# Kernel tuning notes

Measured on AMD Instinct MI355X. Metric: run time of the kernel, lower is better.

## Reference

```python
import jax, jax.numpy as jnp
import numpy as np

# irrep blocks for 0e+1o+2e: dims 1, 3, 5 (total D=9)
BLOCKS = [(0, 1), (1, 4), (4, 9)]

def block_linear(x, W):
    # x: [N, C, 9], W: [3, C, C] -- e3nn Linear mixes channels within each irrep block
    outs = [jnp.einsum('ncd,cq->nqd', x[..., s:e], W[l]) for l, (s, e) in enumerate(BLOCKS)]
    return jnp.concatenate(outs, axis=-1)

def setup_inputs() -> dict:
    key = jax.random.key(0)
    ks = jax.random.split(key, 14)
    N, E, C, D, B, H, Z = 16384, 262144, 32, 9, 8, 64, 4
    inp = {
        'node_feats': jax.random.normal(ks[0], (N, C, D), jnp.float32),
        'node_attrs': jax.random.uniform(ks[1], (N, Z), jnp.float32),
        'edge_feats': jax.random.normal(ks[2], (E, B), jnp.float32),
        'edge_sh': jax.random.normal(ks[3], (E, D), jnp.float32),
        'cutoff': jax.random.uniform(ks[4], (E, 1), jnp.float32),
        # learned params
        'W_up': jax.random.normal(ks[5], (3, C, C), jnp.float32) / np.float32(np.sqrt(C)),
        'W1': jax.random.normal(ks[6], (B, H), jnp.float32) / np.float32(np.sqrt(B)),
        'W2': jax.random.normal(ks[7], (H, H), jnp.float32) / np.float32(np.sqrt(H)),
        'W3': jax.random.normal(ks[8], (H, C), jnp.float32) / np.float32(np.sqrt(H)),
        'W_lin': jax.random.normal(ks[9], (3, C, C), jnp.float32) / np.float32(np.sqrt(C)),
        'W_sc': jax.random.normal(ks[10], (Z, 3, C, C), jnp.float32) / np.float32(np.sqrt(C)),
        # fixed Clebsch-Gordan-like coupling tensor (constant structure of the TP)
        'CG': jax.random.normal(ks[11], (D, D, D), jnp.float32) / np.float32(D),
        'edge_src': jax.random.randint(ks[12], (E,), 0, N, jnp.int32),
        'edge_dst': jax.random.randint(ks[13], (E,), 0, N, jnp.int32),
    }
    return inp

def reference(node_feats, node_attrs, edge_feats, edge_sh, cutoff,
              W_up, W1, W2, W3, W_lin, W_sc, CG, edge_src, edge_dst):
    N = node_feats.shape[0]
    avg_num_neighbors = 16.0
    # linear_up: per-irrep channel mixing
    x = block_linear(node_feats, W_up)
    # radial MLP -> per-edge tensor-product weights, gated by cutoff
    h = jax.nn.silu(edge_feats @ W1)
    h = jax.nn.silu(h @ W2)
    w = (h @ W3) * cutoff  # [E, C]
    # gather source node feats, weighted equivariant tensor product per edge
    xs = x[edge_src]  # [E, C, D]
    m_ij = jnp.einsum('eci,ej,ijk,ec->eck', xs, edge_sh, CG, w)  # [E, C, D]
    # scatter-sum aggregation into destination nodes
    m_i = jax.ops.segment_sum(m_ij, edge_dst, num_segments=N)  # [N, C, D]
    # output linear + neighbor normalization
    m_i = block_linear(m_i, W_lin) / avg_num_neighbors
    # element-dependent self-connection from current message
    W_node = jnp.einsum('nz,zlcq->nlcq', node_attrs, W_sc)  # [N, 3, C, C]
    scs = jnp.concatenate(
        [jnp.einsum('ncd,ncq->nqd', m_i[..., s:e], W_node[:, l]) for l, (s, e) in enumerate(BLOCKS)],
        axis=-1)
    return (m_i, scs)
```

## Files before the change

kernel.cpp:

```cpp
#include <hip/hip_runtime.h>
#include <cstdint>

#define CC 32
#define DD 9
#define CD 288
#define BB 8
#define HH 64
#define ZZ 4
#define NB 8

typedef __attribute__((ext_vector_type(8))) short bf16x8;
typedef __attribute__((ext_vector_type(4))) float f32x4;
typedef __attribute__((ext_vector_type(2))) float f32x2;

__device__ __forceinline__ float silu_f(float v) {
  return v / (1.0f + __expf(-v));
}

__device__ __forceinline__ int blk_of(int d) { return d == 0 ? 0 : (d < 4 ? 1 : 2); }

__device__ __forceinline__ unsigned int f2bf(float f) {
  unsigned int u = __float_as_uint(f);
  return (u + 0x7fffu + ((u >> 16) & 1u)) >> 16;
}
__device__ __forceinline__ float bf_lo(unsigned int u) { return __uint_as_float(u << 16); }
__device__ __forceinline__ float bf_hi(unsigned int u) { return __uint_as_float(u & 0xffff0000u); }

__global__ __launch_bounds__(256) void k_zero(float* __restrict__ p, int n) {
  int i = blockIdx.x * 256 + threadIdx.x;
  if (i < n) p[i] = 0.0f;
}

__global__ __launch_bounds__(256) void k_hist(const int* __restrict__ edst,
                                              int* __restrict__ deg, int E) {
  int e = blockIdx.x * 256 + threadIdx.x;
  if (e < E) atomicAdd(&deg[edst[e]], 1);
}

__global__ __launch_bounds__(1024) void k_scan(const int* __restrict__ deg,
                                               int* __restrict__ offs,
                                               int* __restrict__ cursor, int N) {
  __shared__ int part[1024];
  int t = threadIdx.x;
  int chunk = (N + 1023) >> 10;
  int base = t * chunk;
  int lim = N - base; if (lim > chunk) lim = chunk; if (lim < 0) lim = 0;
  int s = 0;
  for (int i = 0; i < lim; ++i) s += deg[base + i];
  part[t] = s;
  __syncthreads();
  for (int off = 1; off < 1024; off <<= 1) {
    int v = part[t];
    int u = (t >= off) ? part[t - off] : 0;
    __syncthreads();
    part[t] = v + u;
    __syncthreads();
  }
  int run = (t == 0) ? 0 : part[t - 1];
  for (int i = 0; i < lim; ++i) {
    offs[base + i] = run;
    cursor[base + i] = run;
    run += deg[base + i];
  }
  if (t == 1023) offs[N] = run;
}

__global__ __launch_bounds__(256) void k_scatter(const int* __restrict__ edst,
                                                 const int* __restrict__ esrc,
                                                 const float* __restrict__ esh,
                                                 int* __restrict__ cursor,
                                                 int* __restrict__ eidx,
                                                 int* __restrict__ srcs,
                                                 unsigned int* __restrict__ esh_p, int E) {
  int e = blockIdx.x * 256 + threadIdx.x;
  if (e < E) {
    int d = edst[e];
    int pos = atomicAdd(&cursor[d], 1);
    eidx[pos] = e;
    srcs[pos] = esrc[e];
    const float* sp = esh + (size_t)e * 9;
    unsigned int* op = esh_p + (size_t)pos * 5;
#pragma unroll
    for (int jj = 0; jj < 5; ++jj) {
      unsigned int lo = f2bf(sp[2 * jj]);
      unsigned int hi = (jj < 4) ? f2bf(sp[2 * jj + 1]) : 0u;
      op[jj] = lo | (hi << 16);
    }
  }
}

__global__ __launch_bounds__(288) void k_linear_up(
    const float* __restrict__ nf, const float* __restrict__ Wup,
    unsigned int* __restrict__ x_p, int N) {
  __shared__ float snf[NB][DD * 36];
  __shared__ float sval[NB][DD][CC];
  int t = threadIdx.x;
  int g = t >> 5, q = t & 31;
  int tc = t / 9, td = t - tc * 9;
  int l0 = blk_of(g);
  float wcol[CC];
#pragma unroll
  for (int c = 0; c < CC; ++c) wcol[c] = Wup[l0 * 1024 + c * 32 + q];
  int n0 = blockIdx.x * NB;
#pragma unroll
  for (int nb = 0; nb < NB; ++nb) {
    if (n0 + nb < N) snf[nb][td * 36 + tc] = nf[(size_t)(n0 + nb) * CD + t];
  }
  __syncthreads();
#pragma unroll
  for (int nb = 0; nb < NB; ++nb) {
    if (n0 + nb >= N) break;
    const float4* rowp = (const float4*)(snf[nb] + g * 36);
    float a0 = 0.f, a1 = 0.f;
#pragma unroll
    for (int c4 = 0; c4 < 8; ++c4) {
      float4 b = rowp[c4];
      a0 += b.x * wcol[c4 * 4 + 0] + b.y * wcol[c4 * 4 + 1];
      a1 += b.z * wcol[c4 * 4 + 2] + b.w * wcol[c4 * 4 + 3];
    }
    sval[nb][g][q] = a0 + a1;
  }
  __syncthreads();
#pragma unroll
  for (int it = 0; it < 5; ++it) {
    int idx = it * 288 + t;
    if (idx < NB * 160) {
      int nb = idx / 160, r = idx - nb * 160;
      int p = r >> 5, c = r & 31;
      if (n0 + nb < N) {
        unsigned int lo = f2bf(sval[nb][2 * p][c]);
        unsigned int hi = (p < 4) ? f2bf(sval[nb][2 * p + 1][c]) : 0u;
        x_p[(size_t)(n0 + nb) * 160 + r] = lo | (hi << 16);
      }
    }
  }
}

__global__ __launch_bounds__(64) void k_mlp_mfma(
    const float* __restrict__ ef, const float* __restrict__ cut,
    const float* __restrict__ W1, const float* __restrict__ W2,
    const float* __restrict__ W3, const int* __restrict__ eidx,
    unsigned int* __restrict__ w_p, int E) {
  __shared__ ushort hbuf[4096];
  __shared__ ushort h2buf[4096];
  __shared__ float scut[64];
  int l = threadIdx.x;
  int h = l >> 4, li = l & 15;
  bf16x8 A2[4][2];
#pragma unroll
  for (int qm = 0; qm < 4; ++qm)
#pragma unroll
    for (int kb = 0; kb < 2; ++kb)
#pragma unroll
      for (int j = 0; j < 8; ++j)
        A2[qm][kb][j] = (short)f2bf(W2[(32 * kb + 8 * h + j) * HH + 16 * qm + li]);
  bf16x8 A3[2][2];
#pragma unroll
  for (int cm = 0; cm < 2; ++cm)
#pragma unroll
    for (int kb = 0; kb < 2; ++kb)
#pragma unroll
      for (int j = 0; j < 8; ++j)
        A3[cm][kb][j] = (short)f2bf(W3[(32 * kb + 8 * h + j) * CC + 16 * cm + li]);

  int ntile = E >> 6;
  for (int tile = blockIdx.x; tile < ntile; tile += gridDim.x) {
    int pos = tile * 64 + l;
    int eo = eidx[pos];
    const float4* efp = (const float4*)(ef + (size_t)eo * BB);
    float4 efa = efp[0];
    float4 efb = efp[1];
    scut[l] = cut[eo];
    float efv[BB] = {efa.x, efa.y, efa.z, efa.w, efb.x, efb.y, efb.z, efb.w};
#pragma unroll
    for (int g = 0; g < 8; ++g) {
      float hv[8];
#pragma unroll
      for (int jj = 0; jj < 8; ++jj) {
        int q = g * 8 + jj;
        float a = 0.f;
#pragma unroll
        for (int kin = 0; kin < BB; ++kin) a += efv[kin] * W1[kin * HH + q];
        hv[jj] = silu_f(a);
      }
      unsigned int d0 = f2bf(hv[0]) | (f2bf(hv[1]) << 16);
      unsigned int d1 = f2bf(hv[2]) | (f2bf(hv[3]) << 16);
      unsigned int d2 = f2bf(hv[4]) | (f2bf(hv[5]) << 16);
      unsigned int d3 = f2bf(hv[6]) | (f2bf(hv[7]) << 16);
      int F = ((l >> 4) * 2 + (g >> 2)) * 4 + (g & 3);
      *(uint4*)&hbuf[(F * 16 + li) * 8] = make_uint4(d0, d1, d2, d3);
    }
    f32x4 acc2[4][4];
#pragma unroll
    for (int qm = 0; qm < 4; ++qm)
#pragma unroll
      for (int nb = 0; nb < 4; ++nb) acc2[qm][nb] = (f32x4){0.f, 0.f, 0.f, 0.f};
#pragma unroll
    for (int nb = 0; nb < 4; ++nb)
#pragma unroll
      for (int kb = 0; kb < 2; ++kb) {
        int F = (nb * 2 + kb) * 4 + h;
        bf16x8 Bf = *(const bf16x8*)&hbuf[(F * 16 + li) * 8];
#pragma unroll
        for (int qm = 0; qm < 4; ++qm)
          acc2[qm][nb] = __builtin_amdgcn_mfma_f32_16x16x32_bf16(
              A2[qm][kb], Bf, acc2[qm][nb], 0, 0, 0);
      }
#pragma unroll
    for (int qm = 0; qm < 4; ++qm)
#pragma unroll
      for (int nb = 0; nb < 4; ++nb) {
        float v0 = silu_f(acc2[qm][nb][0]);
        float v1 = silu_f(acc2[qm][nb][1]);
        float v2 = silu_f(acc2[qm][nb][2]);
        float v3 = silu_f(acc2[qm][nb][3]);
        unsigned int lo = f2bf(v0) | (f2bf(v1) << 16);
        unsigned int hi = f2bf(v2) | (f2bf(v3) << 16);
        int G = (nb * 2 + (qm >> 1)) * 4 + ((2 * qm + (h >> 1)) & 3);
        *(uint2*)&h2buf[(G * 16 + li) * 8 + (h & 1) * 4] = make_uint2(lo, hi);
      }
    f32x4 acc3[2][4];
#pragma unroll
    for (int cm = 0; cm < 2; ++cm)
#pragma unroll
      for (int nb = 0; nb < 4; ++nb) acc3[cm][nb] = (f32x4){0.f, 0.f, 0.f, 0.f};
#pragma unroll
    for (int nb = 0; nb < 4; ++nb)
#pragma unroll
      for (int kb = 0; kb < 2; ++kb) {
        int G = (nb * 2 + kb) * 4 + h;
        bf16x8 Bf = *(const bf16x8*)&h2buf[(G * 16 + li) * 8];
#pragma unroll
        for (int cm = 0; cm < 2; ++cm)
          acc3[cm][nb] = __builtin_amdgcn_mfma_f32_16x16x32_bf16(
              A3[cm][kb], Bf, acc3[cm][nb], 0, 0, 0);
      }
#pragma unroll
    for (int nb = 0; nb < 4; ++nb) {
      float cv = scut[16 * nb + li];
#pragma unroll
      for (int cm = 0; cm < 2; ++cm) {
        unsigned int lo = f2bf(acc3[cm][nb][0] * cv) | (f2bf(acc3[cm][nb][1] * cv) << 16);
        unsigned int hi = f2bf(acc3[cm][nb][2] * cv) | (f2bf(acc3[cm][nb][3] * cv) << 16);
        *(uint2*)&w_p[(size_t)(tile * 64 + 16 * nb + li) * 16 + 8 * cm + 2 * h] =
            make_uint2(lo, hi);
      }
    }
  }
}

__global__ __launch_bounds__(256) void k_gather(
    const unsigned int* __restrict__ x_p, const unsigned int* __restrict__ w_p,
    const unsigned int* __restrict__ esh_p, const float* __restrict__ CG,
    const int* __restrict__ offs, const int* __restrict__ srcs,
    float* __restrict__ mpre, int N) {
  int wid = (blockIdx.x * 256 + threadIdx.x) >> 6;
  if (wid >= N) return;
  int lane = threadIdx.x & 63;
  int h = lane >> 5, c = lane & 31;
  int beg = offs[wid], end = offs[wid + 1];
  f32x2 Pp[36];
  float P8[9];
#pragma unroll
  for (int i = 0; i < 36; ++i) Pp[i] = (f32x2){0.f, 0.f};
#pragma unroll
  for (int i = 0; i < 9; ++i) P8[i] = 0.f;

  bool okc;
  unsigned int wu_c;
  unsigned int shd_c[5];
  unsigned int xd_c[5];
  {
    int p = beg + h;
    okc = p < end;
    int pp = okc ? p : beg;
    int s = srcs[pp];
    wu_c = w_p[(size_t)pp * 16 + (c >> 1)];
    const unsigned int* shp = esh_p + (size_t)pp * 5;
#pragma unroll
    for (int j = 0; j < 5; ++j) shd_c[j] = shp[j];
    const unsigned int* xp = x_p + (size_t)s * 160 + c;
    xd_c[0] = xp[0]; xd_c[1] = xp[32]; xd_c[2] = xp[64]; xd_c[3] = xp[96]; xd_c[4] = xp[128];
  }

  for (int p0 = beg; p0 < end; p0 += 2) {
    int pn = p0 + 2 + h;
    bool okn = pn < end;
    int ppn = okn ? pn : beg;
    int s_n = srcs[ppn];
    unsigned int wu_n = w_p[(size_t)ppn * 16 + (c >> 1)];
    unsigned int shd_n[5];
    {
      const unsigned int* shp = esh_p + (size_t)ppn * 5;
#pragma unroll
      for (int j = 0; j < 5; ++j) shd_n[j] = shp[j];
    }
    unsigned int xd_n[5];
    {
      const unsigned int* xp = x_p + (size_t)s_n * 160 + c;
      xd_n[0] = xp[0]; xd_n[1] = xp[32]; xd_n[2] = xp[64]; xd_n[3] = xp[96]; xd_n[4] = xp[128];
    }
    float wc = okc ? ((c & 1) ? bf_hi(wu_c) : bf_lo(wu_c)) : 0.f;
    f32x2 sh2[4];
    sh2[0] = (f32x2){bf_lo(shd_c[0]), bf_hi(shd_c[0])};
    sh2[1] = (f32x2){bf_lo(shd_c[1]), bf_hi(shd_c[1])};
    sh2[2] = (f32x2){bf_lo(shd_c[2]), bf_hi(shd_c[2])};
    sh2[3] = (f32x2){bf_lo(shd_c[3]), bf_hi(shd_c[3])};
    float sh8 = bf_lo(shd_c[4]);
    float xs[DD];
    xs[0] = bf_lo(xd_c[0]); xs[1] = bf_hi(xd_c[0]);
    xs[2] = bf_lo(xd_c[1]); xs[3] = bf_hi(xd_c[1]);
    xs[4] = bf_lo(xd_c[2]); xs[5] = bf_hi(xd_c[2]);
    xs[6] = bf_lo(xd_c[3]); xs[7] = bf_hi(xd_c[3]);
    xs[8] = bf_lo(xd_c[4]);
#pragma unroll
    for (int i = 0; i < DD; ++i) {
      float t = wc * xs[i];
      f32x2 t2 = (f32x2){t, t};
#pragma unroll
      for (int jp = 0; jp < 4; ++jp) Pp[i * 4 + jp] = t2 * sh2[jp] + Pp[i * 4 + jp];
      P8[i] += t * sh8;
    }
    okc = okn;
    wu_c = wu_n;
#pragma unroll
    for (int j = 0; j < 5; ++j) { shd_c[j] = shd_n[j]; xd_c[j] = xd_n[j]; }
  }

  f32x2 m2[4];
  float m8 = 0.f;
#pragma unroll
  for (int kp = 0; kp < 4; ++kp) m2[kp] = (f32x2){0.f, 0.f};
#pragma unroll
  for (int i = 0; i < DD; ++i) {
#pragma unroll
    for (int j = 0; j < DD; ++j) {
      float p = (j < 8) ? ((j & 1) ? Pp[i * 4 + (j >> 1)].y : Pp[i * 4 + (j >> 1)].x)
                        : P8[i];
      f32x2 p2 = (f32x2){p, p};
      const float* cgr = CG + i * 81 + j * DD;
#pragma unroll
      for (int kp = 0; kp < 4; ++kp) {
        f32x2 cg2 = (f32x2){cgr[2 * kp], cgr[2 * kp + 1]};
        m2[kp] = p2 * cg2 + m2[kp];
      }
      m8 += p * cgr[8];
    }
  }
  float m[DD];
  m[0] = m2[0].x; m[1] = m2[0].y;
  m[2] = m2[1].x; m[3] = m2[1].y;
  m[4] = m2[2].x; m[5] = m2[2].y;
  m[6] = m2[3].x; m[7] = m2[3].y;
  m[8] = m8;
#pragma unroll
  for (int k = 0; k < DD; ++k) m[k] += __shfl_xor(m[k], 32);
  if (h == 0) {
    float* mp = mpre + (size_t)wid * CD + c;
#pragma unroll
    for (int k = 0; k < DD; ++k) mp[k * 32] = m[k];
  }
}

__global__ __launch_bounds__(288, 1) void k_out(
    const float* __restrict__ attrs, const float* __restrict__ Wlin,
    const float* __restrict__ Wsc,
    float* __restrict__ out1, float* __restrict__ out2, int N) {
  __shared__ float smp[NB][CD];
  __shared__ float smt[NB][CD];
  __shared__ float sres1[NB * CD];
  __shared__ float sres2[NB * CD];
  int t = threadIdx.x;
  int g = t >> 5, q = t & 31;
  int l0 = blk_of(g);
  float wl[CC];
#pragma unroll
  for (int c = 0; c < CC; ++c) wl[c] = Wlin[l0 * 1024 + c * 32 + q];
  float ws0[CC], ws1[CC], ws2[CC], ws3[CC];
#pragma unroll
  for (int c = 0; c < CC; ++c) {
    ws0[c] = Wsc[0 * 3072 + l0 * 1024 + c * 32 + q];
    ws1[c] = Wsc[1 * 3072 + l0 * 1024 + c * 32 + q];
    ws2[c] = Wsc[2 * 3072 + l0 * 1024 + c * 32 + q];
    ws3[c] = Wsc[3 * 3072 + l0 * 1024 + c * 32 + q];
  }
  int nbat = (N + NB - 1) / NB;
  int b = blockIdx.x;
  float r[NB];
  if (b < nbat) {
#pragma unroll
    for (int nb = 0; nb < NB; ++nb) r[nb] = out2[(size_t)(b * NB + nb) * CD + t];
  }
  for (; b < nbat; b += gridDim.x) {
    int n0 = b * NB;
    __syncthreads();
#pragma unroll
    for (int nb = 0; nb < NB; ++nb) smp[nb][t] = r[nb];
    float4 av[NB];
#pragma unroll
    for (int nb = 0; nb < NB; ++nb) av[nb] = ((const float4*)attrs)[n0 + nb];
    __syncthreads();
    int b2 = b + gridDim.x;
    if (b2 < nbat) {
#pragma unroll
      for (int nb = 0; nb < NB; ++nb) r[nb] = out2[(size_t)(b2 * NB + nb) * CD + t];
    }
#pragma unroll
    for (int nb = 0; nb < NB; ++nb) {
      const float4* rowp = (const float4*)(smp[nb] + g * 32);
      float b0 = 0.f, b1 = 0.f;
#pragma unroll
      for (int c4 = 0; c4 < 8; ++c4) {
        float4 bb = rowp[c4];
        b0 += bb.x * wl[c4 * 4 + 0] + bb.y * wl[c4 * 4 + 1];
        b1 += bb.z * wl[c4 * 4 + 2] + bb.w * wl[c4 * 4 + 3];
      }
      float v = (b0 + b1) * (1.0f / 16.0f);
      smt[nb][t] = v;
      sres1[nb * CD + q * DD + g] = v;
    }
    __syncthreads();
#pragma unroll
    for (int nb = 0; nb < NB; ++nb) {
      const float4* rowp = (const float4*)(smt[nb] + g * 32);
      float z0 = 0.f, z1 = 0.f, z2 = 0.f, z3 = 0.f;
#pragma unroll
      for (int c4 = 0; c4 < 8; ++c4) {
        float4 bb = rowp[c4];
#pragma unroll
        for (int j = 0; j < 4; ++j) {
          float bv = (j == 0) ? bb.x : (j == 1) ? bb.y : (j == 2) ? bb.z : bb.w;
          int c = c4 * 4 + j;
          z0 += bv * ws0[c];
          z1 += bv * ws1[c];
          z2 += bv * ws2[c];
          z3 += bv * ws3[c];
        }
      }
      float4 a = av[nb];
      sres2[nb * CD + q * DD + g] = a.x * z0 + a.y * z1 + a.z * z2 + a.w * z3;
    }
    __syncthreads();
#pragma unroll
    for (int rr = 0; rr < (NB * 72) / 288; ++rr) {
      int s = rr * 288 + t;
      int nb = s / 72, idx = s - nb * 72;
      ((float4*)(out1 + (size_t)(n0 + nb) * CD))[idx] = ((const float4*)sres1)[s];
      ((float4*)(out2 + (size_t)(n0 + nb) * CD))[idx] = ((const float4*)sres2)[s];
    }
  }
}

extern "C" void kernel_launch(void* const* d_in, const int* in_sizes, int n_in,
                              void* d_out, int out_size, void* d_ws, size_t ws_size,
                              hipStream_t stream) {
  const float* nf    = (const float*)d_in[0];
  const float* attrs = (const float*)d_in[1];
  const float* ef    = (const float*)d_in[2];
  const float* esh   = (const float*)d_in[3];
  const float* cutv  = (const float*)d_in[4];
  const float* Wup   = (const float*)d_in[5];
  const float* W1    = (const float*)d_in[6];
  const float* W2    = (const float*)d_in[7];
  const float* W3    = (const float*)d_in[8];
  const float* Wlin  = (const float*)d_in[9];
  const float* Wsc   = (const float*)d_in[10];
  const float* CG    = (const float*)d_in[11];
  const int* esrc    = (const int*)d_in[12];
  const int* edst    = (const int*)d_in[13];
  int N = in_sizes[0] / CD;
  int E = in_sizes[12];
  float* out1 = (float*)d_out;
  float* out2 = out1 + (size_t)N * CD;

  unsigned int* x_p   = (unsigned int*)d_ws;
  unsigned int* w_p   = x_p + (size_t)N * 160;
  unsigned int* esh_p = w_p + (size_t)E * 16;
  int* deg     = (int*)(esh_p + (size_t)E * 5);
  int* offs    = deg + N;
  int* cursor  = offs + N + 1;
  int* eidx    = cursor + N;
  int* srcs    = eidx + E;

  int nblk = (N + NB - 1) / NB;
  k_zero<<<(N + 255) / 256, 256, 0, stream>>>((float*)deg, N);
  k_hist<<<(E + 255) / 256, 256, 0, stream>>>(edst, deg, E);
  k_scan<<<1, 1024, 0, stream>>>(deg, offs, cursor, N);
  k_scatter<<<(E + 255) / 256, 256, 0, stream>>>(edst, esrc, esh, cursor, eidx, srcs, esh_p, E);
  k_linear_up<<<nblk, 288, 0, stream>>>(nf, Wup, x_p, N);
  k_mlp_mfma<<<4096, 64, 0, stream>>>(ef, cutv, W1, W2, W3, eidx, w_p, E);
  k_gather<<<(N + 3) / 4, 256, 0, stream>>>(x_p, w_p, esh_p, CG, offs, srcs, out2, N);
  k_out<<<512, 288, 0, stream>>>(attrs, Wlin, Wsc, out1, out2, N);
}
```

Baseline: 235.6 us.

## Make linear_up persistent with register prefetch and merge MLP LDS buffers

k_linear_up becomes a persistent kernel on a fixed 512-block grid. Each block loops over node batches, and the next batch's node features are prefetched into registers while the current batch is computed. This amortizes the per-block load of the weight columns and overlaps global loads with compute. Separately, the MLP kernel reuses one shared buffer for both hidden activations, halving its LDS footprint to allow higher occupancy; this relies on the ordering of reads and writes across the single-wavefront block.

```diff
diff --git a/kernel.cpp b/kernel.cpp
--- a/kernel.cpp
+++ b/kernel.cpp
@@ -89,7 +89,7 @@
   }
 }
 
-__global__ __launch_bounds__(288) void k_linear_up(
+__global__ __launch_bounds__(288, 1) void k_linear_up(
     const float* __restrict__ nf, const float* __restrict__ Wup,
     unsigned int* __restrict__ x_p, int N) {
   __shared__ float snf[NB][DD * 36];
@@ -101,36 +101,54 @@
   float wcol[CC];
 #pragma unroll
   for (int c = 0; c < CC; ++c) wcol[c] = Wup[l0 * 1024 + c * 32 + q];
-  int n0 = blockIdx.x * NB;
-#pragma unroll
-  for (int nb = 0; nb < NB; ++nb) {
-    if (n0 + nb < N) snf[nb][td * 36 + tc] = nf[(size_t)(n0 + nb) * CD + t];
-  }
-  __syncthreads();
-#pragma unroll
-  for (int nb = 0; nb < NB; ++nb) {
-    if (n0 + nb >= N) break;
-    const float4* rowp = (const float4*)(snf[nb] + g * 36);
-    float a0 = 0.f, a1 = 0.f;
-#pragma unroll
-    for (int c4 = 0; c4 < 8; ++c4) {
-      float4 b = rowp[c4];
-      a0 += b.x * wcol[c4 * 4 + 0] + b.y * wcol[c4 * 4 + 1];
-      a1 += b.z * wcol[c4 * 4 + 2] + b.w * wcol[c4 * 4 + 3];
-    }
-    sval[nb][g][q] = a0 + a1;
-  }
-  __syncthreads();
-#pragma unroll
-  for (int it = 0; it < 5; ++it) {
-    int idx = it * 288 + t;
-    if (idx < NB * 160) {
-      int nb = idx / 160, r = idx - nb * 160;
-      int p = r >> 5, c = r & 31;
-      if (n0 + nb < N) {
-        unsigned int lo = f2bf(sval[nb][2 * p][c]);
-        unsigned int hi = (p < 4) ? f2bf(sval[nb][2 * p + 1][c]) : 0u;
-        x_p[(size_t)(n0 + nb) * 160 + r] = lo | (hi << 16);
+  int nbat = (N + NB - 1) / NB;
+  int b = blockIdx.x;
+  float r[NB];
+  if (b < nbat) {
+#pragma unroll
+    for (int nb = 0; nb < NB; ++nb) {
+      int n = b * NB + nb; if (n >= N) n = N - 1;
+      r[nb] = nf[(size_t)n * CD + t];
+    }
+  }
+  for (; b < nbat; b += gridDim.x) {
+    int n0 = b * NB;
+    __syncthreads();
+#pragma unroll
+    for (int nb = 0; nb < NB; ++nb) snf[nb][td * 36 + tc] = r[nb];
+    __syncthreads();
+    int b2 = b + gridDim.x;
+    if (b2 < nbat) {
+#pragma unroll
+      for (int nb = 0; nb < NB; ++nb) {
+        int n = b2 * NB + nb; if (n >= N) n = N - 1;
+        r[nb] = nf[(size_t)n * CD + t];
+      }
+    }
+#pragma unroll
+    for (int nb = 0; nb < NB; ++nb) {
+      const float4* rowp = (const float4*)(snf[nb] + g * 36);
+      float a0 = 0.f, a1 = 0.f;
+#pragma unroll
+      for (int c4 = 0; c4 < 8; ++c4) {
+        float4 bb = rowp[c4];
+        a0 += bb.x * wcol[c4 * 4 + 0] + bb.y * wcol[c4 * 4 + 1];
+        a1 += bb.z * wcol[c4 * 4 + 2] + bb.w * wcol[c4 * 4 + 3];
+      }
+      sval[nb][g][q] = a0 + a1;
+    }
+    __syncthreads();
+#pragma unroll
+    for (int it = 0; it < 5; ++it) {
+      int idx = it * 288 + t;
+      if (idx < NB * 160) {
+        int nb = idx / 160, rr = idx - nb * 160;
+        int p = rr >> 5, c = rr & 31;
+        if (n0 + nb < N) {
+          unsigned int lo = f2bf(sval[nb][2 * p][c]);
+          unsigned int hi = (p < 4) ? f2bf(sval[nb][2 * p + 1][c]) : 0u;
+          x_p[(size_t)(n0 + nb) * 160 + rr] = lo | (hi << 16);
+        }
       }
     }
   }
@@ -141,8 +159,7 @@
     const float* __restrict__ W1, const float* __restrict__ W2,
     const float* __restrict__ W3, const int* __restrict__ eidx,
     unsigned int* __restrict__ w_p, int E) {
-  __shared__ ushort hbuf[4096];
-  __shared__ ushort h2buf[4096];
+  __shared__ ushort buf[4096];
   __shared__ float scut[64];
   int l = threadIdx.x;
   int h = l >> 4, li = l & 15;
@@ -188,7 +205,7 @@
       unsigned int d2 = f2bf(hv[4]) | (f2bf(hv[5]) << 16);
       unsigned int d3 = f2bf(hv[6]) | (f2bf(hv[7]) << 16);
       int F = ((l >> 4) * 2 + (g >> 2)) * 4 + (g & 3);
-      *(uint4*)&hbuf[(F * 16 + li) * 8] = make_uint4(d0, d1, d2, d3);
+      *(uint4*)&buf[(F * 16 + li) * 8] = make_uint4(d0, d1, d2, d3);
     }
     f32x4 acc2[4][4];
 #pragma unroll
@@ -200,7 +217,7 @@
 #pragma unroll
       for (int kb = 0; kb < 2; ++kb) {
         int F = (nb * 2 + kb) * 4 + h;
-        bf16x8 Bf = *(const bf16x8*)&hbuf[(F * 16 + li) * 8];
+        bf16x8 Bf = *(const bf16x8*)&buf[(F * 16 + li) * 8];
 #pragma unroll
         for (int qm = 0; qm < 4; ++qm)
           acc2[qm][nb] = __builtin_amdgcn_mfma_f32_16x16x32_bf16(
@@ -217,7 +234,7 @@
         unsigned int lo = f2bf(v0) | (f2bf(v1) << 16);
         unsigned int hi = f2bf(v2) | (f2bf(v3) << 16);
         int G = (nb * 2 + (qm >> 1)) * 4 + ((2 * qm + (h >> 1)) & 3);
-        *(uint2*)&h2buf[(G * 16 + li) * 8 + (h & 1) * 4] = make_uint2(lo, hi);
+        *(uint2*)&buf[(G * 16 + li) * 8 + (h & 1) * 4] = make_uint2(lo, hi);
       }
     f32x4 acc3[2][4];
 #pragma unroll
@@ -229,7 +246,7 @@
 #pragma unroll
       for (int kb = 0; kb < 2; ++kb) {
         int G = (nb * 2 + kb) * 4 + h;
-        bf16x8 Bf = *(const bf16x8*)&h2buf[(G * 16 + li) * 8];
+        bf16x8 Bf = *(const bf16x8*)&buf[(G * 16 + li) * 8];
 #pragma unroll
         for (int cm = 0; cm < 2; ++cm)
           acc3[cm][nb] = __builtin_amdgcn_mfma_f32_16x16x32_bf16(
@@ -482,12 +499,11 @@
   int* eidx    = cursor + N;
   int* srcs    = eidx + E;
 
-  int nblk = (N + NB - 1) / NB;
   k_zero<<<(N + 255) / 256, 256, 0, stream>>>((float*)deg, N);
   k_hist<<<(E + 255) / 256, 256, 0, stream>>>(edst, deg, E);
   k_scan<<<1, 1024, 0, stream>>>(deg, offs, cursor, N);
   k_scatter<<<(E + 255) / 256, 256, 0, stream>>>(edst, esrc, esh, cursor, eidx, srcs, esh_p, E);
-  k_linear_up<<<nblk, 288, 0, stream>>>(nf, Wup, x_p, N);
+  k_linear_up<<<512, 288, 0, stream>>>(nf, Wup, x_p, N);
   k_mlp_mfma<<<4096, 64, 0, stream>>>(ef, cutv, W1, W2, W3, eidx, w_p, E);
   k_gather<<<(N + 3) / 4, 256, 0, stream>>>(x_p, w_p, esh_p, CG, offs, srcs, out2, N);
   k_out<<<512, 288, 0, stream>>>(attrs, Wlin, Wsc, out1, out2, N);
```

Measured after the change: 236.5 us (median of 2 runs). No clear change (+0.4%).
